# Optimization experiments

Measured on AMD Instinct MI355X. Metric: run time of the kernel, lower is better.

Reference implementation:

```python
import jax, jax.numpy as jnp
import numpy as np

B, L, H, NH, P = 4, 1024, 1024, 16, 2048
HD = H // NH


def setup_inputs() -> dict:
    key = jax.random.key(0)
    ks = jax.random.split(key, 6)
    x = jax.random.normal(ks[0], (B, L, H), dtype=jnp.float32)
    # torch.nn.Linear weights are [out, in]
    Wqkv = jax.random.normal(ks[1], (3 * H, H), dtype=jnp.float32) * 0.02
    bqkv = jnp.zeros((3 * H,), dtype=jnp.float32)
    Wo = jax.random.normal(ks[2], (H, H), dtype=jnp.float32) * 0.02
    bo = jnp.zeros((H,), dtype=jnp.float32)
    Er = jax.random.normal(ks[3], (NH, P, HD), dtype=jnp.float32)
    # causal mask: True where attention is disallowed (masked_fill semantics)
    mask = jnp.triu(jnp.ones((L, L), dtype=bool), k=1)
    return {"x": x, "mask": mask, "Wqkv": Wqkv, "bqkv": bqkv,
            "Wo": Wo, "bo": bo, "Er": Er}


def reference(x, mask, Wqkv, bqkv, Wo, bo, Er):
    b, l, d = x.shape
    nh, p, hd = Er.shape
    qkv = x @ Wqkv.T + bqkv                      # [b, l, 3d]
    q, k, v = jnp.split(qkv, 3, axis=-1)
    q = q.reshape(b, l, nh, hd).transpose(0, 2, 1, 3)   # [b, nh, l, hd]
    k = k.reshape(b, l, nh, hd).transpose(0, 2, 1, 3)
    v = v.reshape(b, l, nh, hd).transpose(0, 2, 1, 3)

    scores = jnp.einsum('bnlh,bnkh->bnlk', q, k) / jnp.sqrt(
        jnp.asarray(hd, dtype=x.dtype))

    # relative positions (j - i), torch negative-index wraparound -> mod p
    pos = jnp.arange(l)
    rel = (pos[None, :] - pos[:, None]) % p      # [l, l] in [0, p)
    # Equivalent to einsum('bnlh,rnlkh->bnlk', q, Er[:, rel][None]) but
    # computed as q @ Er^T over all positions then gathered (same math,
    # avoids materializing the [nh, l, l, hd] tensor).
    QEr_full = jnp.einsum('bnlh,nph->bnlp', q, Er)       # [b, nh, l, p]
    i_idx = pos[:, None]                          # broadcasts with rel
    QEr = QEr_full[:, :, i_idx, rel]              # [b, nh, l, l]

    a = scores + QEr
    a = jnp.where(mask, -jnp.inf, a)
    a = jax.nn.softmax(a, axis=-1)                # dropout: eval mode (identity)

    out = jnp.einsum('bnlk,bnkh->bnlh', a, v)     # [b, nh, l, hd]
    out = out.transpose(0, 2, 1, 3).reshape(b, l, d)
    return out @ Wo.T + bo
```

## Files before the change

### kernel.cpp

```cpp
#include <hip/hip_runtime.h>

typedef unsigned short u16;
typedef __bf16 bf16x8 __attribute__((ext_vector_type(8)));
typedef unsigned short u16x8 __attribute__((ext_vector_type(8)));
typedef float f32x4 __attribute__((ext_vector_type(4)));

#define MFMA16(a, b, c) __builtin_amdgcn_mfma_f32_16x16x32_bf16((a), (b), (c), 0, 0, 0)

#define WAVE_LDS_FENCE() do { \
  asm volatile("s_waitcnt lgkmcnt(0)" ::: "memory"); \
  __builtin_amdgcn_sched_barrier(0); \
} while (0)

__device__ __forceinline__ u16 f2b(float f) {
  unsigned u = __float_as_uint(f);
  u += 0x7fffu + ((u >> 16) & 1u);
  return (u16)(u >> 16);
}
__device__ __forceinline__ float b2f(u16 h) {
  return __uint_as_float(((unsigned)h) << 16);
}

__global__ void cvt_bf16(const float* __restrict__ src, u16* __restrict__ dst, int n4) {
  int i = blockIdx.x * blockDim.x + threadIdx.x;
  if (i >= n4) return;
  float4 v = *(const float4*)(src + (size_t)i * 4);
  *(ushort4*)(dst + (size_t)i * 4) = make_ushort4(f2b(v.x), f2b(v.y), f2b(v.z), f2b(v.w));
}

__global__ void build_F(const float* __restrict__ Er, u16* __restrict__ Fb) {
  int i = blockIdx.x * blockDim.x + threadIdx.x;
  int base = i * 4;
  int d = base & 63;
  int m = (base >> 6) & 1023;
  int n = base >> 16;
  int sm = (2048 - m) & 2047;
  float4 v = *(const float4*)(Er + ((size_t)(n * 2048 + sm) * 64 + d));
  *(ushort4*)(Fb + (size_t)base) = make_ushort4(f2b(v.x), f2b(v.y), f2b(v.z), f2b(v.w));
}

__global__ __launch_bounds__(256) void transpose_v(const u16* __restrict__ V, u16* __restrict__ Vt) {
  __shared__ u16 T[4096];
  const int bn = blockIdx.x, i0 = blockIdx.y * 64;
  const int t = threadIdx.x;
#pragma unroll
  for (int s = 0; s < 2; ++s) {
    int ch = t + 256 * s;
    int i = ch >> 3, c = ch & 7;
    u16x8 v = *(const u16x8*)&V[(size_t)((bn << 10) + i0 + i) * 64 + c * 8];
#pragma unroll
    for (int e = 0; e < 8; ++e) {
      int d = c * 8 + e;
      T[d * 64 + ((((i >> 3) ^ (d & 7) ^ ((d >> 3) & 7)) & 7) << 3) + (i & 7)] = v[e];
    }
  }
  __syncthreads();
#pragma unroll
  for (int s = 0; s < 2; ++s) {
    int ch = t + 256 * s;
    int d = ch >> 3, cc = ch & 7;
    u16x8 o = *(const u16x8*)&T[d * 64 + (((cc ^ (d & 7) ^ ((d >> 3) & 7)) & 7) << 3)];
    *(u16x8*)&Vt[(size_t)((bn << 6) + d) * 1024 + i0 + cc * 8] = o;
  }
}

__global__ __launch_bounds__(256) void gemm_qkv(const u16* __restrict__ A, const u16* __restrict__ Bw,
                                                const float* __restrict__ bias,
                                                u16* __restrict__ Qo, u16* __restrict__ Ko,
                                                u16* __restrict__ Vo) {
  __shared__ u16 As[4][128][8];
  __shared__ u16 Bs[4][128][8];
  const int m0 = blockIdx.y * 128, n0 = blockIdx.x * 128;
  const int t = threadIdx.x, lane = t & 63, w = t >> 6;
  const int wr = w >> 1, wc = w & 1;
  const int l16 = lane & 15, lg = lane >> 4;
  f32x4 acc[4][4] = {};
  const int ch0 = t * 2, ch1 = t * 2 + 1;
  const int r0 = ch0 >> 2, g0 = ch0 & 3, r1 = ch1 >> 2, g1 = ch1 & 3;

  u16x8 pa0 = *(const u16x8*)&A[(size_t)(m0 + r0) * 1024 + g0 * 8];
  u16x8 pa1 = *(const u16x8*)&A[(size_t)(m0 + r1) * 1024 + g1 * 8];
  u16x8 pb0 = *(const u16x8*)&Bw[(size_t)(n0 + r0) * 1024 + g0 * 8];
  u16x8 pb1 = *(const u16x8*)&Bw[(size_t)(n0 + r1) * 1024 + g1 * 8];

  for (int k0 = 0; k0 < 1024; k0 += 32) {
    *(u16x8*)&As[g0][r0][0] = pa0;
    *(u16x8*)&As[g1][r1][0] = pa1;
    *(u16x8*)&Bs[g0][r0][0] = pb0;
    *(u16x8*)&Bs[g1][r1][0] = pb1;
    __syncthreads();
    if (k0 + 32 < 1024) {
      int k1 = k0 + 32;
      pa0 = *(const u16x8*)&A[(size_t)(m0 + r0) * 1024 + k1 + g0 * 8];
      pa1 = *(const u16x8*)&A[(size_t)(m0 + r1) * 1024 + k1 + g1 * 8];
      pb0 = *(const u16x8*)&Bw[(size_t)(n0 + r0) * 1024 + k1 + g0 * 8];
      pb1 = *(const u16x8*)&Bw[(size_t)(n0 + r1) * 1024 + k1 + g1 * 8];
    }
    bf16x8 af[4], bfr[4];
#pragma unroll
    for (int m = 0; m < 4; ++m) af[m] = *(const bf16x8*)&As[lg][wr * 64 + m * 16 + l16][0];
#pragma unroll
    for (int n = 0; n < 4; ++n) bfr[n] = *(const bf16x8*)&Bs[lg][wc * 64 + n * 16 + l16][0];
#pragma unroll
    for (int m = 0; m < 4; ++m)
#pragma unroll
      for (int n = 0; n < 4; ++n) acc[m][n] = MFMA16(af[m], bfr[n], acc[m][n]);
    __syncthreads();
  }

#pragma unroll
  for (int n = 0; n < 4; ++n) {
    int col = n0 + wc * 64 + n * 16 + l16;
    float bq = bias[col];
    int which = col >> 10;
    int h = col & 1023;
    int head = h >> 6, d = h & 63;
    u16* dst = which == 0 ? Qo : (which == 1 ? Ko : Vo);
    float scale = which == 1 ? 0.125f : 1.0f;
#pragma unroll
    for (int m = 0; m < 4; ++m) {
#pragma unroll
      for (int r = 0; r < 4; ++r) {
        int row = m0 + wr * 64 + m * 16 + lg * 4 + r;
        int b = row >> 10, ii = row & 1023;
        float v = (acc[m][n][r] + bq) * scale;
        dst[(size_t)(((b * 16 + head) << 10) + ii) * 64 + d] = f2b(v);
      }
    }
  }
}

__global__ __launch_bounds__(256) void gemm_out(const u16* __restrict__ A, const u16* __restrict__ Bw,
                                                const float* __restrict__ bias, float* __restrict__ Co) {
  __shared__ u16 As[4][128][8];
  __shared__ u16 Bs[4][128][8];
  const int m0 = blockIdx.y * 128, n0 = blockIdx.x * 128;
  const int t = threadIdx.x, lane = t & 63, w = t >> 6;
  const int wr = w >> 1, wc = w & 1;
  const int l16 = lane & 15, lg = lane >> 4;
  f32x4 acc[4][4] = {};
  const int ch0 = t * 2, ch1 = t * 2 + 1;
  const int r0 = ch0 >> 2, g0 = ch0 & 3, r1 = ch1 >> 2, g1 = ch1 & 3;

  u16x8 pa0 = *(const u16x8*)&A[(size_t)(m0 + r0) * 1024 + g0 * 8];
  u16x8 pa1 = *(const u16x8*)&A[(size_t)(m0 + r1) * 1024 + g1 * 8];
  u16x8 pb0 = *(const u16x8*)&Bw[(size_t)(n0 + r0) * 1024 + g0 * 8];
  u16x8 pb1 = *(const u16x8*)&Bw[(size_t)(n0 + r1) * 1024 + g1 * 8];

  for (int k0 = 0; k0 < 1024; k0 += 32) {
    *(u16x8*)&As[g0][r0][0] = pa0;
    *(u16x8*)&As[g1][r1][0] = pa1;
    *(u16x8*)&Bs[g0][r0][0] = pb0;
    *(u16x8*)&Bs[g1][r1][0] = pb1;
    __syncthreads();
    if (k0 + 32 < 1024) {
      int k1 = k0 + 32;
      pa0 = *(const u16x8*)&A[(size_t)(m0 + r0) * 1024 + k1 + g0 * 8];
      pa1 = *(const u16x8*)&A[(size_t)(m0 + r1) * 1024 + k1 + g1 * 8];
      pb0 = *(const u16x8*)&Bw[(size_t)(n0 + r0) * 1024 + k1 + g0 * 8];
      pb1 = *(const u16x8*)&Bw[(size_t)(n0 + r1) * 1024 + k1 + g1 * 8];
    }
    bf16x8 af[4], bfr[4];
#pragma unroll
    for (int m = 0; m < 4; ++m) af[m] = *(const bf16x8*)&As[lg][wr * 64 + m * 16 + l16][0];
#pragma unroll
    for (int n = 0; n < 4; ++n) bfr[n] = *(const bf16x8*)&Bs[lg][wc * 64 + n * 16 + l16][0];
#pragma unroll
    for (int m = 0; m < 4; ++m)
#pragma unroll
      for (int n = 0; n < 4; ++n) acc[m][n] = MFMA16(af[m], bfr[n], acc[m][n]);
    __syncthreads();
  }

#pragma unroll
  for (int n = 0; n < 4; ++n) {
    int col = n0 + wc * 64 + n * 16 + l16;
    float bq = bias[col];
#pragma unroll
    for (int m = 0; m < 4; ++m) {
#pragma unroll
      for (int r = 0; r < 4; ++r) {
        int row = m0 + wr * 64 + m * 16 + lg * 4 + r;
        Co[(size_t)row * 1024 + col] = acc[m][n][r] + bq;
      }
    }
  }
}

__global__ __launch_bounds__(256) void attn_kernel(const u16* __restrict__ Qg, const u16* __restrict__ Kg,
                                                   const u16* __restrict__ Vtg, const u16* __restrict__ Fg,
                                                   u16* __restrict__ AO) {
  __shared__ u16 Kl[4096];
  __shared__ u16 Vl[4096];
  __shared__ u16 Fl[8192];
  __shared__ u16 Bnd[4][16][84];
  __shared__ u16 Pl[4][1024];

  const int bn = blockIdx.x;
  const int b = bn >> 4, n = bn & 15;
  const int qt = 15 - (int)blockIdx.y;
  const int i0 = qt * 64;
  const int t = threadIdx.x, lane = t & 63, w = t >> 6;
  const int l16 = lane & 15, lg = lane >> 4;

  bf16x8 qf[2];
  {
    const u16* qp = &Qg[(size_t)((bn << 10) + i0 + (w << 4) + l16) * 64 + lg * 8];
    qf[0] = *(const bf16x8*)qp;
    qf[1] = *(const bf16x8*)(qp + 32);
  }

  float mrun[4], lrun[4];
  f32x4 ao[4] = {};
#pragma unroll
  for (int r = 0; r < 4; ++r) { mrun[r] = -3.0e38f; lrun[r] = 0.0f; }

  for (int jt = 0; jt <= qt; ++jt) {
    const int j0 = jt * 64;
    const int mbase = i0 - j0 - 63;
    const bool diag = (jt == qt);

#pragma unroll
    for (int s = 0; s < 2; ++s) {
      int ch = t + 256 * s;
      int r = ch >> 3, c = ch & 7;
      u16x8 kv = *(const u16x8*)&Kg[(size_t)((bn << 10) + j0 + r) * 64 + c * 8];
      *(u16x8*)&Kl[r * 64 + (((c ^ (r & 7)) & 7) << 3)] = kv;
      u16x8 vv = *(const u16x8*)&Vtg[(size_t)((bn << 6) + r) * 1024 + j0 + c * 8];
      *(u16x8*)&Vl[r * 64 + (((c ^ (r & 7)) & 7) << 3)] = vv;
    }
#pragma unroll
    for (int s = 0; s < 4; ++s) {
      int ch = t + 256 * s;
      int r = ch >> 3, c = ch & 7;
      int mrow = mbase + r;
      mrow = mrow < 0 ? 0 : (mrow > 1023 ? 1023 : mrow);
      u16x8 fv = *(const u16x8*)&Fg[(size_t)((n << 10) + mrow) * 64 + c * 8];
      *(u16x8*)&Fl[r * 64 + (((c ^ (r & 7)) & 7) << 3)] = fv;
    }
    __syncthreads();

    f32x4 sc[4] = {};
#pragma unroll
    for (int kk = 0; kk < 2; ++kk)
#pragma unroll
      for (int nn = 0; nn < 4; ++nn) {
        int jr = nn * 16 + l16;
        bf16x8 kb = *(const bf16x8*)&Kl[jr * 64 + ((((lg + 4 * kk) ^ (jr & 7)) & 7) << 3)];
        sc[nn] = MFMA16(qf[kk], kb, sc[nn]);
      }
    f32x4 bb[5] = {};
#pragma unroll
    for (int kk = 0; kk < 2; ++kk)
#pragma unroll
      for (int ct = 0; ct < 5; ++ct) {
        int trow = (w << 4) + ct * 16 + l16;
        bf16x8 fb = *(const bf16x8*)&Fl[trow * 64 + ((((lg + 4 * kk) ^ (trow & 7)) & 7) << 3)];
        bb[ct] = MFMA16(qf[kk], fb, bb[ct]);
      }
#pragma unroll
    for (int ct = 0; ct < 5; ++ct)
#pragma unroll
      for (int r = 0; r < 4; ++r)
        Bnd[w][lg * 4 + r][ct * 16 + l16] = f2b(bb[ct][r]);
    WAVE_LDS_FENCE();

    const unsigned* bw = (const unsigned*)&Bnd[w][0][0];
    float pv[4][4];
#pragma unroll
    for (int r = 0; r < 4; ++r) {
      int il = lg * 4 + r;
      int c0 = il - l16 + 63;
      int u0 = il * 84 + c0;
      int sh = (u0 & 1) << 4;
      float stmp[4];
      float mx = -3.0e38f;
#pragma unroll
      for (int nn = 0; nn < 4; ++nn) {
        unsigned dv = bw[(u0 >> 1) - 8 * nn];
        float s = sc[nn][r] + b2f((u16)((dv >> sh) & 0xffffu));
        if (diag && (c0 - 16 * nn + (w << 4) < 63)) s = -1.0e30f;
        stmp[nn] = s;
        mx = fmaxf(mx, s);
      }
#pragma unroll
      for (int off = 1; off < 16; off <<= 1) mx = fmaxf(mx, __shfl_xor(mx, off));
      float mnew = fmaxf(mrun[r], mx);
      float scl = __expf(mrun[r] - mnew);
      float rs = 0.0f;
#pragma unroll
      for (int nn = 0; nn < 4; ++nn) {
        pv[nn][r] = __expf(stmp[nn] - mnew);
        rs += pv[nn][r];
      }
#pragma unroll
      for (int off = 1; off < 16; off <<= 1) rs += __shfl_xor(rs, off);
      lrun[r] = lrun[r] * scl + rs;
      mrun[r] = mnew;
#pragma unroll
      for (int nd = 0; nd < 4; ++nd) ao[nd][r] *= scl;
    }

#pragma unroll
    for (int nn = 0; nn < 4; ++nn)
#pragma unroll
      for (int r = 0; r < 4; ++r) {
        int i = lg * 4 + r, j = nn * 16 + l16;
        Pl[w][i * 64 + ((((j >> 3) ^ (i & 7)) & 7) << 3) + (j & 7)] = f2b(pv[nn][r]);
      }
    WAVE_LDS_FENCE();
#pragma unroll
    for (int kk = 0; kk < 2; ++kk) {
      bf16x8 pa = *(const bf16x8*)&Pl[w][l16 * 64 + ((((lg + 4 * kk) ^ (l16 & 7)) & 7) << 3)];
#pragma unroll
      for (int nd = 0; nd < 4; ++nd) {
        int dr = nd * 16 + l16;
        bf16x8 vb = *(const bf16x8*)&Vl[dr * 64 + ((((lg + 4 * kk) ^ (dr & 7)) & 7) << 3)];
        ao[nd] = MFMA16(pa, vb, ao[nd]);
      }
    }
    __syncthreads();
  }

#pragma unroll
  for (int nd = 0; nd < 4; ++nd)
#pragma unroll
    for (int r = 0; r < 4; ++r) {
      int i = i0 + (w << 4) + lg * 4 + r;
      int d = nd * 16 + l16;
      float v = ao[nd][r] / lrun[r];
      AO[(size_t)((b << 10) + i) * 1024 + n * 64 + d] = f2b(v);
    }
}

extern "C" void kernel_launch(void* const* d_in, const int* in_sizes, int n_in,
                              void* d_out, int out_size, void* d_ws, size_t ws_size,
                              hipStream_t stream) {
  (void)in_sizes; (void)n_in; (void)out_size; (void)ws_size;
  const float* x    = (const float*)d_in[0];
  const float* Wqkv = (const float*)d_in[2];
  const float* bqkv = (const float*)d_in[3];
  const float* Wo   = (const float*)d_in[4];
  const float* bo   = (const float*)d_in[5];
  const float* Er   = (const float*)d_in[6];
  float* out = (float*)d_out;

  char* p = (char*)d_ws;
  u16* xb    = (u16*)p; p += (size_t)4096 * 1024 * 2;
  u16* wqkvb = (u16*)p; p += (size_t)3072 * 1024 * 2;
  u16* wob   = (u16*)p; p += (size_t)1024 * 1024 * 2;
  u16* Fb    = (u16*)p; p += (size_t)16 * 1024 * 64 * 2;
  u16* Qb    = (u16*)p; p += (size_t)64 * 1024 * 64 * 2;
  u16* Kb    = (u16*)p; p += (size_t)64 * 1024 * 64 * 2;
  u16* Vb    = (u16*)p; p += (size_t)64 * 1024 * 64 * 2;
  u16* Vtb   = (u16*)p; p += (size_t)64 * 1024 * 64 * 2;
  u16* AO    = (u16*)p; p += (size_t)4096 * 1024 * 2;

  cvt_bf16<<<4096, 256, 0, stream>>>(x, xb, 1048576);
  cvt_bf16<<<3072, 256, 0, stream>>>(Wqkv, wqkvb, 786432);
  cvt_bf16<<<1024, 256, 0, stream>>>(Wo, wob, 262144);
  build_F<<<1024, 256, 0, stream>>>(Er, Fb);
  gemm_qkv<<<dim3(24, 32), 256, 0, stream>>>(xb, wqkvb, bqkv, Qb, Kb, Vb);
  transpose_v<<<dim3(64, 16), 256, 0, stream>>>(Vb, Vtb);
  attn_kernel<<<dim3(64, 16), 256, 0, stream>>>(Qb, Kb, Vtb, Fb, AO);
  gemm_out<<<dim3(8, 32), 256, 0, stream>>>(AO, wob, bo, out);
}
```

Before: 154.3 us.

## Use direct global-to-LDS loads in GEMMs and prefetch attention tiles into registers

Both GEMMs drop their register-staged prefetch and instead use global_load_lds to fill a 64-wide K slice per iteration, halving the number of barriers per K. The attention kernel now prefetches the next K/V/F tile into registers while computing the current tile. It also defers the row-sum cross-lane reduction until after the loop, keeping per-lane partial sums. The GEMM path loses its overlap of global loads with MFMA, since loads are now issued and waited on within the same iteration.

After: 174.5 us. +13.1%, slower.

```diff
diff --git a/kernel.cpp b/kernel.cpp
--- a/kernel.cpp
+++ b/kernel.cpp
@@ -11,6 +11,10 @@
   asm volatile("s_waitcnt lgkmcnt(0)" ::: "memory"); \
   __builtin_amdgcn_sched_barrier(0); \
 } while (0)
+
+#define GLDS(gp, lp) __builtin_amdgcn_global_load_lds( \
+    (const __attribute__((address_space(1))) unsigned int*)(gp), \
+    (__attribute__((address_space(3))) unsigned int*)(lp), 16, 0, 0)
 
 __device__ __forceinline__ u16 f2b(float f) {
   unsigned u = __float_as_uint(f);
@@ -68,43 +72,35 @@
                                                 const float* __restrict__ bias,
                                                 u16* __restrict__ Qo, u16* __restrict__ Ko,
                                                 u16* __restrict__ Vo) {
-  __shared__ u16 As[4][128][8];
-  __shared__ u16 Bs[4][128][8];
+  __shared__ u16 As[8][128][8];
+  __shared__ u16 Bs[8][128][8];
   const int m0 = blockIdx.y * 128, n0 = blockIdx.x * 128;
   const int t = threadIdx.x, lane = t & 63, w = t >> 6;
   const int wr = w >> 1, wc = w & 1;
   const int l16 = lane & 15, lg = lane >> 4;
   f32x4 acc[4][4] = {};
-  const int ch0 = t * 2, ch1 = t * 2 + 1;
-  const int r0 = ch0 >> 2, g0 = ch0 & 3, r1 = ch1 >> 2, g1 = ch1 & 3;
-
-  u16x8 pa0 = *(const u16x8*)&A[(size_t)(m0 + r0) * 1024 + g0 * 8];
-  u16x8 pa1 = *(const u16x8*)&A[(size_t)(m0 + r1) * 1024 + g1 * 8];
-  u16x8 pb0 = *(const u16x8*)&Bw[(size_t)(n0 + r0) * 1024 + g0 * 8];
-  u16x8 pb1 = *(const u16x8*)&Bw[(size_t)(n0 + r1) * 1024 + g1 * 8];
-
-  for (int k0 = 0; k0 < 1024; k0 += 32) {
-    *(u16x8*)&As[g0][r0][0] = pa0;
-    *(u16x8*)&As[g1][r1][0] = pa1;
-    *(u16x8*)&Bs[g0][r0][0] = pb0;
-    *(u16x8*)&Bs[g1][r1][0] = pb1;
-    __syncthreads();
-    if (k0 + 32 < 1024) {
-      int k1 = k0 + 32;
-      pa0 = *(const u16x8*)&A[(size_t)(m0 + r0) * 1024 + k1 + g0 * 8];
-      pa1 = *(const u16x8*)&A[(size_t)(m0 + r1) * 1024 + k1 + g1 * 8];
-      pb0 = *(const u16x8*)&Bw[(size_t)(n0 + r0) * 1024 + k1 + g0 * 8];
-      pb1 = *(const u16x8*)&Bw[(size_t)(n0 + r1) * 1024 + k1 + g1 * 8];
-    }
-    bf16x8 af[4], bfr[4];
-#pragma unroll
-    for (int m = 0; m < 4; ++m) af[m] = *(const bf16x8*)&As[lg][wr * 64 + m * 16 + l16][0];
-#pragma unroll
-    for (int n = 0; n < 4; ++n) bfr[n] = *(const bf16x8*)&Bs[lg][wc * 64 + n * 16 + l16][0];
-#pragma unroll
-    for (int m = 0; m < 4; ++m)
-#pragma unroll
-      for (int n = 0; n < 4; ++n) acc[m][n] = MFMA16(af[m], bfr[n], acc[m][n]);
+
+  for (int k0 = 0; k0 < 1024; k0 += 64) {
+#pragma unroll
+    for (int s = 0; s < 4; ++s) {
+      int c = t + 256 * s;
+      int r = c & 127, g = c >> 7;
+      GLDS(&A[(size_t)(m0 + r) * 1024 + k0 + g * 8], &As[g][r][0]);
+      GLDS(&Bw[(size_t)(n0 + r) * 1024 + k0 + g * 8], &Bs[g][r][0]);
+    }
+    __syncthreads();
+#pragma unroll
+    for (int kk = 0; kk < 2; ++kk) {
+      bf16x8 af[4], bfr[4];
+#pragma unroll
+      for (int m = 0; m < 4; ++m) af[m] = *(const bf16x8*)&As[lg + 4 * kk][wr * 64 + m * 16 + l16][0];
+#pragma unroll
+      for (int n = 0; n < 4; ++n) bfr[n] = *(const bf16x8*)&Bs[lg + 4 * kk][wc * 64 + n * 16 + l16][0];
+#pragma unroll
+      for (int m = 0; m < 4; ++m)
+#pragma unroll
+        for (int n = 0; n < 4; ++n) acc[m][n] = MFMA16(af[m], bfr[n], acc[m][n]);
+    }
     __syncthreads();
   }
 
@@ -132,43 +128,35 @@
 
 __global__ __launch_bounds__(256) void gemm_out(const u16* __restrict__ A, const u16* __restrict__ Bw,
                                                 const float* __restrict__ bias, float* __restrict__ Co) {
-  __shared__ u16 As[4][128][8];
-  __shared__ u16 Bs[4][128][8];
+  __shared__ u16 As[8][128][8];
+  __shared__ u16 Bs[8][128][8];
   const int m0 = blockIdx.y * 128, n0 = blockIdx.x * 128;
   const int t = threadIdx.x, lane = t & 63, w = t >> 6;
   const int wr = w >> 1, wc = w & 1;
   const int l16 = lane & 15, lg = lane >> 4;
   f32x4 acc[4][4] = {};
-  const int ch0 = t * 2, ch1 = t * 2 + 1;
-  const int r0 = ch0 >> 2, g0 = ch0 & 3, r1 = ch1 >> 2, g1 = ch1 & 3;
-
-  u16x8 pa0 = *(const u16x8*)&A[(size_t)(m0 + r0) * 1024 + g0 * 8];
-  u16x8 pa1 = *(const u16x8*)&A[(size_t)(m0 + r1) * 1024 + g1 * 8];
-  u16x8 pb0 = *(const u16x8*)&Bw[(size_t)(n0 + r0) * 1024 + g0 * 8];
-  u16x8 pb1 = *(const u16x8*)&Bw[(size_t)(n0 + r1) * 1024 + g1 * 8];
-
-  for (int k0 = 0; k0 < 1024; k0 += 32) {
-    *(u16x8*)&As[g0][r0][0] = pa0;
-    *(u16x8*)&As[g1][r1][0] = pa1;
-    *(u16x8*)&Bs[g0][r0][0] = pb0;
-    *(u16x8*)&Bs[g1][r1][0] = pb1;
-    __syncthreads();
-    if (k0 + 32 < 1024) {
-      int k1 = k0 + 32;
-      pa0 = *(const u16x8*)&A[(size_t)(m0 + r0) * 1024 + k1 + g0 * 8];
-      pa1 = *(const u16x8*)&A[(size_t)(m0 + r1) * 1024 + k1 + g1 * 8];
-      pb0 = *(const u16x8*)&Bw[(size_t)(n0 + r0) * 1024 + k1 + g0 * 8];
-      pb1 = *(const u16x8*)&Bw[(size_t)(n0 + r1) * 1024 + k1 + g1 * 8];
-    }
-    bf16x8 af[4], bfr[4];
-#pragma unroll
-    for (int m = 0; m < 4; ++m) af[m] = *(const bf16x8*)&As[lg][wr * 64 + m * 16 + l16][0];
-#pragma unroll
-    for (int n = 0; n < 4; ++n) bfr[n] = *(const bf16x8*)&Bs[lg][wc * 64 + n * 16 + l16][0];
-#pragma unroll
-    for (int m = 0; m < 4; ++m)
-#pragma unroll
-      for (int n = 0; n < 4; ++n) acc[m][n] = MFMA16(af[m], bfr[n], acc[m][n]);
+
+  for (int k0 = 0; k0 < 1024; k0 += 64) {
+#pragma unroll
+    for (int s = 0; s < 4; ++s) {
+      int c = t + 256 * s;
+      int r = c & 127, g = c >> 7;
+      GLDS(&A[(size_t)(m0 + r) * 1024 + k0 + g * 8], &As[g][r][0]);
+      GLDS(&Bw[(size_t)(n0 + r) * 1024 + k0 + g * 8], &Bs[g][r][0]);
+    }
+    __syncthreads();
+#pragma unroll
+    for (int kk = 0; kk < 2; ++kk) {
+      bf16x8 af[4], bfr[4];
+#pragma unroll
+      for (int m = 0; m < 4; ++m) af[m] = *(const bf16x8*)&As[lg + 4 * kk][wr * 64 + m * 16 + l16][0];
+#pragma unroll
+      for (int n = 0; n < 4; ++n) bfr[n] = *(const bf16x8*)&Bs[lg + 4 * kk][wc * 64 + n * 16 + l16][0];
+#pragma unroll
+      for (int m = 0; m < 4; ++m)
+#pragma unroll
+        for (int n = 0; n < 4; ++n) acc[m][n] = MFMA16(af[m], bfr[n], acc[m][n]);
+    }
     __syncthreads();
   }
 
@@ -203,6 +191,11 @@
   const int t = threadIdx.x, lane = t & 63, w = t >> 6;
   const int l16 = lane & 15, lg = lane >> 4;
 
+  const int rr0 = t >> 3, cc0 = t & 7;
+  const int rr1 = (t + 256) >> 3, cc1 = t & 7;
+  const int rr2 = (t + 512) >> 3, cc2 = t & 7;
+  const int rr3 = (t + 768) >> 3, cc3 = t & 7;
+
   bf16x8 qf[2];
   {
     const u16* qp = &Qg[(size_t)((bn << 10) + i0 + (w << 4) + l16) * 64 + lg * 8];
@@ -210,35 +203,45 @@
     qf[1] = *(const bf16x8*)(qp + 32);
   }
 
-  float mrun[4], lrun[4];
+  float mrun[4], lsum[4];
   f32x4 ao[4] = {};
 #pragma unroll
-  for (int r = 0; r < 4; ++r) { mrun[r] = -3.0e38f; lrun[r] = 0.0f; }
+  for (int r = 0; r < 4; ++r) { mrun[r] = -3.0e38f; lsum[r] = 0.0f; }
+
+  u16x8 rk0, rk1, rv0, rv1, rf0, rf1, rf2, rf3;
+
+#define LOAD_STAGE(jt_) do { \
+    int j0_ = (jt_) * 64, mb_ = i0 - j0_ - 63; \
+    rk0 = *(const u16x8*)&Kg[(size_t)((bn << 10) + j0_ + rr0) * 64 + cc0 * 8]; \
+    rk1 = *(const u16x8*)&Kg[(size_t)((bn << 10) + j0_ + rr1) * 64 + cc1 * 8]; \
+    rv0 = *(const u16x8*)&Vtg[(size_t)((bn << 6) + rr0) * 1024 + j0_ + cc0 * 8]; \
+    rv1 = *(const u16x8*)&Vtg[(size_t)((bn << 6) + rr1) * 1024 + j0_ + cc1 * 8]; \
+    int m0_ = mb_ + rr0; m0_ = m0_ < 0 ? 0 : (m0_ > 1023 ? 1023 : m0_); \
+    int m1_ = mb_ + rr1; m1_ = m1_ < 0 ? 0 : (m1_ > 1023 ? 1023 : m1_); \
+    int m2_ = mb_ + rr2; m2_ = m2_ < 0 ? 0 : (m2_ > 1023 ? 1023 : m2_); \
+    int m3_ = mb_ + rr3; m3_ = m3_ < 0 ? 0 : (m3_ > 1023 ? 1023 : m3_); \
+    rf0 = *(const u16x8*)&Fg[(size_t)((n << 10) + m0_) * 64 + cc0 * 8]; \
+    rf1 = *(const u16x8*)&Fg[(size_t)((n << 10) + m1_) * 64 + cc1 * 8]; \
+    rf2 = *(const u16x8*)&Fg[(size_t)((n << 10) + m2_) * 64 + cc2 * 8]; \
+    rf3 = *(const u16x8*)&Fg[(size_t)((n << 10) + m3_) * 64 + cc3 * 8]; \
+  } while (0)
+
+  LOAD_STAGE(0);
 
   for (int jt = 0; jt <= qt; ++jt) {
-    const int j0 = jt * 64;
-    const int mbase = i0 - j0 - 63;
     const bool diag = (jt == qt);
 
-#pragma unroll
-    for (int s = 0; s < 2; ++s) {
-      int ch = t + 256 * s;
-      int r = ch >> 3, c = ch & 7;
-      u16x8 kv = *(const u16x8*)&Kg[(size_t)((bn << 10) + j0 + r) * 64 + c * 8];
-      *(u16x8*)&Kl[r * 64 + (((c ^ (r & 7)) & 7) << 3)] = kv;
-      u16x8 vv = *(const u16x8*)&Vtg[(size_t)((bn << 6) + r) * 1024 + j0 + c * 8];
-      *(u16x8*)&Vl[r * 64 + (((c ^ (r & 7)) & 7) << 3)] = vv;
-    }
-#pragma unroll
-    for (int s = 0; s < 4; ++s) {
-      int ch = t + 256 * s;
-      int r = ch >> 3, c = ch & 7;
-      int mrow = mbase + r;
-      mrow = mrow < 0 ? 0 : (mrow > 1023 ? 1023 : mrow);
-      u16x8 fv = *(const u16x8*)&Fg[(size_t)((n << 10) + mrow) * 64 + c * 8];
-      *(u16x8*)&Fl[r * 64 + (((c ^ (r & 7)) & 7) << 3)] = fv;
-    }
-    __syncthreads();
+    *(u16x8*)&Kl[rr0 * 64 + (((cc0 ^ (rr0 & 7)) & 7) << 3)] = rk0;
+    *(u16x8*)&Kl[rr1 * 64 + (((cc1 ^ (rr1 & 7)) & 7) << 3)] = rk1;
+    *(u16x8*)&Vl[rr0 * 64 + (((cc0 ^ (rr0 & 7)) & 7) << 3)] = rv0;
+    *(u16x8*)&Vl[rr1 * 64 + (((cc1 ^ (rr1 & 7)) & 7) << 3)] = rv1;
+    *(u16x8*)&Fl[rr0 * 64 + (((cc0 ^ (rr0 & 7)) & 7) << 3)] = rf0;
+    *(u16x8*)&Fl[rr1 * 64 + (((cc1 ^ (rr1 & 7)) & 7) << 3)] = rf1;
+    *(u16x8*)&Fl[rr2 * 64 + (((cc2 ^ (rr2 & 7)) & 7) << 3)] = rf2;
+    *(u16x8*)&Fl[rr3 * 64 + (((cc3 ^ (rr3 & 7)) & 7) << 3)] = rf3;
+    __syncthreads();
+
+    if (jt < qt) LOAD_STAGE(jt + 1);
 
     f32x4 sc[4] = {};
 #pragma unroll
@@ -293,9 +296,7 @@
         pv[nn][r] = __expf(stmp[nn] - mnew);
         rs += pv[nn][r];
       }
-#pragma unroll
-      for (int off = 1; off < 16; off <<= 1) rs += __shfl_xor(rs, off);
-      lrun[r] = lrun[r] * scl + rs;
+      lsum[r] = lsum[r] * scl + rs;
       mrun[r] = mnew;
 #pragma unroll
       for (int nd = 0; nd < 4; ++nd) ao[nd][r] *= scl;
@@ -323,14 +324,20 @@
   }
 
 #pragma unroll
+  for (int r = 0; r < 4; ++r)
+#pragma unroll
+    for (int off = 1; off < 16; off <<= 1) lsum[r] += __shfl_xor(lsum[r], off);
+
+#pragma unroll
   for (int nd = 0; nd < 4; ++nd)
 #pragma unroll
     for (int r = 0; r < 4; ++r) {
       int i = i0 + (w << 4) + lg * 4 + r;
       int d = nd * 16 + l16;
-      float v = ao[nd][r] / lrun[r];
+      float v = ao[nd][r] / lsum[r];
       AO[(size_t)((b << 10) + i) * 1024 + n * 64 + d] = f2b(v);
     }
+#undef LOAD_STAGE
 }
 
 extern "C" void kernel_launch(void* const* d_in, const int* in_sizes, int n_in,
```
